# Kernel tuning notes

Measured on AMD Instinct MI355X. Metric: run time of the kernel, lower is better.

## Reference

```python
import jax, jax.numpy as jnp
import numpy as np

BN_EPS = 1e-3  # Keras BatchNormalization default epsilon


def batchnorm(x, gamma, beta):
    # axis=2 channel BN with training=True: batch stats over (batch, seq)
    m = jnp.mean(x, axis=(0, 1))
    v = jnp.var(x, axis=(0, 1))
    return gamma * (x - m) * jax.lax.rsqrt(v + BN_EPS) + beta


def setup_inputs() -> dict:
    key = jax.random.key(0)
    ks = jax.random.split(key, 8)
    B, L, Din, D, S = 8, 512, 64, 1024, 2
    s = 0.02
    return {
        "x": jax.random.normal(ks[0], (B, L, Din), jnp.float32),
        "W_embed": jax.random.normal(ks[1], (Din, D), jnp.float32) * s,
        "bn1_gamma": jnp.ones((D,), jnp.float32),
        "bn1_beta": jnp.zeros((D,), jnp.float32),
        "Wq": jax.random.normal(ks[2], (S, D, D), jnp.float32) * s,
        "bq": jnp.zeros((S, D), jnp.float32),
        "Wk": jax.random.normal(ks[3], (S, D, D), jnp.float32) * s,
        "bk": jnp.zeros((S, D), jnp.float32),
        "Wv": jax.random.normal(ks[4], (S, D, D), jnp.float32) * s,
        "bv": jnp.zeros((S, D), jnp.float32),
        "bn_gamma": jnp.ones((S, D), jnp.float32),
        "bn_beta": jnp.zeros((S, D), jnp.float32),
        "Wc1": jax.random.normal(ks[5], (S, D, D), jnp.float32) * s,
        "bc1": jnp.zeros((S, D), jnp.float32),
        "bn2_gamma": jnp.ones((S, D), jnp.float32),
        "bn2_beta": jnp.zeros((S, D), jnp.float32),
        "num_heads": 16,
    }


def reference(x, W_embed, bn1_gamma, bn1_beta, Wq, bq, Wk, bk, Wv, bv,
              bn_gamma, bn_beta, Wc1, bc1, bn2_gamma, bn2_beta, num_heads):
    # embedding: kernel-1 conv1d == matmul, then BN (training stats)
    enc = batchnorm(jnp.einsum('bli,id->bld', x, W_embed), bn1_gamma, bn1_beta)
    S = Wq.shape[0]
    B, L, D = enc.shape
    h = num_heads
    dh = D // h
    scale = 1.0 / (dh ** 0.5)
    for i in range(S):
        # relu-activated Q/K/V projections (Dense(..., activation=relu))
        q = jax.nn.relu(jnp.einsum('bld,de->ble', enc, Wq[i]) + bq[i])
        k = jax.nn.relu(jnp.einsum('bld,de->ble', enc, Wk[i]) + bk[i])
        v = jax.nn.relu(jnp.einsum('bld,de->ble', enc, Wv[i]) + bv[i])
        # split/concat head trick == reshape to [B, L, h, dh]
        qh = q.reshape(B, L, h, dh)
        kh = k.reshape(B, L, h, dh)
        vh = v.reshape(B, L, h, dh)
        scores = jnp.einsum('blhd,bmhd->bhlm', qh, kh) * scale
        attn = jax.nn.softmax(scores, axis=-1)
        out = jnp.einsum('bhlm,bmhd->blhd', attn, vh).reshape(B, L, D)
        enc = batchnorm(out + enc, bn_gamma[i], bn_beta[i])
        # feedforward: source applies conv1 TWICE (conv2 unused) — faithful
        f = jax.nn.relu(jnp.einsum('bld,de->ble', enc, Wc1[i]) + bc1[i])
        f = jax.nn.relu(jnp.einsum('bld,de->ble', f, Wc1[i]) + bc1[i])
        enc = batchnorm(f + enc, bn2_gamma[i], bn2_beta[i])
    return enc
```

## Files before the change

kernel.cpp:

```cpp
#include <hip/hip_runtime.h>
#include <hip/hip_bf16.h>
#include <cstddef>

#define D_MODEL 1024
#define M_ROWS  4096
#define BN_EPS  1e-3f
#define C_EXP2  0.18033688011112042f
#define INV_N   (1.0f / 4096.0f)

typedef __attribute__((ext_vector_type(8))) short short8;
typedef __attribute__((ext_vector_type(4))) short short4v;
typedef __attribute__((ext_vector_type(8))) unsigned short ushortx8;
typedef __attribute__((ext_vector_type(4))) float f32x4;

__device__ __forceinline__ unsigned short f2bf(float f) {
    __hip_bfloat16 h = __float2bfloat16(f);
    return *reinterpret_cast<unsigned short*>(&h);
}
__device__ __forceinline__ float bf2f(unsigned short u) {
    return __uint_as_float(((unsigned)u) << 16);
}
__device__ __forceinline__ unsigned int cvt_pk_bf16(float lo, float hi) {
    unsigned int r;
    asm volatile("v_cvt_pk_bf16_f32 %0, %1, %2" : "=v"(r) : "v"(lo), "v"(hi));
    return r;
}

template<int MODE>
__global__ __launch_bounds__(256)
void gemm_bf16_kernel(const unsigned short* __restrict__ A,
                      const unsigned short* __restrict__ Bt,
                      const float* __restrict__ b0, const float* __restrict__ b1,
                      const float* __restrict__ b2,
                      unsigned short* __restrict__ Cout,
                      const unsigned short* __restrict__ resid,
                      float* __restrict__ accp, int N, int Kd) {
    __shared__ unsigned short As[2][128 * 32];
    __shared__ unsigned short Bs[2][128 * 32];
    const int tid = threadIdx.x;
    const int lane = tid & 63;
    const int w = tid >> 6;
    const int wr = w >> 1, wc = w & 1;
    const int rowBase = blockIdx.y * 128;
    const int colBase = blockIdx.x * 128;

    const int chunk0 = w * 64 + lane;
    const int r0 = chunk0 >> 2;
    const int c0 = (chunk0 & 3) ^ ((r0 >> 1) & 3);
    const int chunk1 = 256 + chunk0;
    const int r1 = chunk1 >> 2;
    const int c1 = (chunk1 & 3) ^ ((r1 >> 1) & 3);
    const size_t aOff0 = (size_t)(rowBase + r0) * Kd + c0 * 8;
    const size_t aOff1 = (size_t)(rowBase + r1) * Kd + c1 * 8;
    const size_t bOff0 = (size_t)(colBase + r0) * Kd + c0 * 8;
    const size_t bOff1 = (size_t)(colBase + r1) * Kd + c1 * 8;
    const int ldsOff0 = (w * 64) * 8;
    const int ldsOff1 = (256 + w * 64) * 8;

    f32x4 acc[4][4];
    #pragma unroll
    for (int m = 0; m < 4; ++m)
        #pragma unroll
        for (int n = 0; n < 4; ++n)
            acc[m][n] = (f32x4){0.f, 0.f, 0.f, 0.f};

    #define STAGE(buf, kt) do {                                                   \
        const int k0_ = (kt) << 5;                                                \
        __builtin_amdgcn_global_load_lds(                                         \
            (const __attribute__((address_space(1))) void*)(A + aOff0 + k0_),     \
            (__attribute__((address_space(3))) void*)(&As[buf][ldsOff0]), 16, 0, 0);\
        __builtin_amdgcn_global_load_lds(                                         \
            (const __attribute__((address_space(1))) void*)(A + aOff1 + k0_),     \
            (__attribute__((address_space(3))) void*)(&As[buf][ldsOff1]), 16, 0, 0);\
        __builtin_amdgcn_global_load_lds(                                         \
            (const __attribute__((address_space(1))) void*)(Bt + bOff0 + k0_),    \
            (__attribute__((address_space(3))) void*)(&Bs[buf][ldsOff0]), 16, 0, 0);\
        __builtin_amdgcn_global_load_lds(                                         \
            (const __attribute__((address_space(1))) void*)(Bt + bOff1 + k0_),    \
            (__attribute__((address_space(3))) void*)(&Bs[buf][ldsOff1]), 16, 0, 0);\
    } while (0)

    const int NT = Kd >> 5;
    STAGE(0, 0);

    const int kb = lane >> 4;
    const int s = kb ^ ((lane >> 1) & 3);
    const int rA = wr * 64 + (lane & 15);
    const int rB = wc * 64 + (lane & 15);

    for (int t = 0; t < NT; ++t) {
        __syncthreads();
        if (t + 1 < NT) STAGE((t + 1) & 1, t + 1);
        const unsigned short* as = As[t & 1];
        const unsigned short* bs = Bs[t & 1];
        short8 a[4], b[4];
        #pragma unroll
        for (int m = 0; m < 4; ++m)
            a[m] = *(const short8*)&as[(rA + m * 16) * 32 + s * 8];
        #pragma unroll
        for (int n = 0; n < 4; ++n)
            b[n] = *(const short8*)&bs[(rB + n * 16) * 32 + s * 8];
        #pragma unroll
        for (int m = 0; m < 4; ++m)
            #pragma unroll
            for (int n = 0; n < 4; ++n)
                acc[m][n] = __builtin_amdgcn_mfma_f32_16x16x32_bf16(
                    a[m], b[n], acc[m][n], 0, 0, 0);
    }
    #undef STAGE

    const int cRow0 = rowBase + wr * 64 + (lane >> 4) * 4;
    const int cCol0 = colBase + wc * 64 + (lane & 15);
    float cs[4] = {}, cq[4] = {};
    #pragma unroll
    for (int n = 0; n < 4; ++n) {
        const int col = cCol0 + n * 16;
        float bv = 0.0f;
        if (MODE != 2) {
            const float* bp = (col < 1024) ? b0 : (col < 2048) ? b1 : b2;
            bv = bp[col & 1023];
        }
        #pragma unroll
        for (int m = 0; m < 4; ++m)
            #pragma unroll
            for (int r = 0; r < 4; ++r) {
                const int row = cRow0 + m * 16 + r;
                float v = acc[m][n][r];
                if (MODE != 2) v = fmaxf(v + bv, 0.0f);
                if (MODE == 1) v += bf2f(resid[(size_t)row * N + col]);
                if (MODE != 0) { cs[n] += v; cq[n] += v * v; }
                Cout[(size_t)row * N + col] = f2bf(v);
            }
    }
    if (MODE != 0) {
        #pragma unroll
        for (int n = 0; n < 4; ++n) {
            cs[n] += __shfl_xor(cs[n], 16); cs[n] += __shfl_xor(cs[n], 32);
            cq[n] += __shfl_xor(cq[n], 16); cq[n] += __shfl_xor(cq[n], 32);
        }
        if (lane < 16) {
            #pragma unroll
            for (int n = 0; n < 4; ++n) {
                const int col = colBase + wc * 64 + lane + n * 16;
                atomicAdd(&accp[col], cs[n]);
                atomicAdd(&accp[D_MODEL + col], cq[n]);
            }
        }
    }
}

__global__ __launch_bounds__(256)
void prep_weights_kernel(const float* __restrict__ Wq, const float* __restrict__ Wk,
                         const float* __restrict__ Wv, const float* __restrict__ Wc1,
                         unsigned short* __restrict__ Wtqkv,
                         unsigned short* __restrict__ Wtc1) {
    const int z = blockIdx.z;
    const int layer = z >> 2, typ = z & 3;
    const size_t wo = (size_t)layer * 1048576;
    const float* src;
    unsigned short* dst;
    if (typ == 0)      { src = Wq + wo;  dst = Wtqkv + layer * 3145728; }
    else if (typ == 1) { src = Wk + wo;  dst = Wtqkv + layer * 3145728 + 1048576; }
    else if (typ == 2) { src = Wv + wo;  dst = Wtqkv + layer * 3145728 + 2097152; }
    else               { src = Wc1 + wo; dst = Wtc1 + layer * 1048576; }
    __shared__ float T[64][65];
    const int tid = threadIdx.x;
    const int kBase = blockIdx.y * 64;
    const int nBase = blockIdx.x * 64;
    const int rr = tid >> 4;
    const int c4 = (tid & 15) * 4;
    #pragma unroll
    for (int i = 0; i < 4; ++i) {
        const int k = i * 16 + rr;
        const float4 v = *reinterpret_cast<const float4*>(
            &src[(size_t)(kBase + k) * 1024 + nBase + c4]);
        T[k][c4] = v.x; T[k][c4 + 1] = v.y; T[k][c4 + 2] = v.z; T[k][c4 + 3] = v.w;
    }
    __syncthreads();
    #pragma unroll
    for (int i = 0; i < 4; ++i) {
        const int n = i * 16 + rr;
        ushort4 o;
        o.x = f2bf(T[c4 + 0][n]); o.y = f2bf(T[c4 + 1][n]);
        o.z = f2bf(T[c4 + 2][n]); o.w = f2bf(T[c4 + 3][n]);
        *reinterpret_cast<ushort4*>(&dst[(size_t)(nBase + n) * 1024 + kBase + c4]) = o;
    }
}

__global__ __launch_bounds__(256)
void prep_misc_kernel(const float* __restrict__ x, const float* __restrict__ Wemb,
                      unsigned short* __restrict__ xbf,
                      unsigned short* __restrict__ Wembt,
                      float* __restrict__ accum) {
    const int b = blockIdx.x;
    const int tid = threadIdx.x;
    if (b < 128) {
        const size_t base = (size_t)b * 2048 + tid * 8;
        const float4 v0 = *reinterpret_cast<const float4*>(&x[base]);
        const float4 v1 = *reinterpret_cast<const float4*>(&x[base + 4]);
        ushortx8 o;
        o[0] = f2bf(v0.x); o[1] = f2bf(v0.y); o[2] = f2bf(v0.z); o[3] = f2bf(v0.w);
        o[4] = f2bf(v1.x); o[5] = f2bf(v1.y); o[6] = f2bf(v1.z); o[7] = f2bf(v1.w);
        *reinterpret_cast<ushortx8*>(&xbf[base]) = o;
    } else if (b < 144) {
        __shared__ float T[64][65];
        const int nBase = (b - 128) * 64;
        const int rr = tid >> 4;
        const int c4 = (tid & 15) * 4;
        #pragma unroll
        for (int i = 0; i < 4; ++i) {
            const int k = i * 16 + rr;
            const float4 v = *reinterpret_cast<const float4*>(
                &Wemb[(size_t)k * 1024 + nBase + c4]);
            T[k][c4] = v.x; T[k][c4 + 1] = v.y; T[k][c4 + 2] = v.z; T[k][c4 + 3] = v.w;
        }
        __syncthreads();
        #pragma unroll
        for (int i = 0; i < 4; ++i) {
            const int n = i * 16 + rr;
            ushort4 o;
            o.x = f2bf(T[c4 + 0][n]); o.y = f2bf(T[c4 + 1][n]);
            o.z = f2bf(T[c4 + 2][n]); o.w = f2bf(T[c4 + 3][n]);
            *reinterpret_cast<ushort4*>(&Wembt[(size_t)(nBase + n) * 64 + c4]) = o;
        }
    } else {
        for (int j = tid; j < 5 * 2048; j += 256) accum[j] = 0.0f;
    }
}

__global__ __launch_bounds__(256)
void attn_kernel(const unsigned short* __restrict__ QKV,
                 const unsigned short* __restrict__ Ebf,
                 unsigned short* __restrict__ Sbf,
                 float* __restrict__ accp) {
    __shared__ unsigned short Qs[128 * 64];
    __shared__ unsigned short Ks[2][64 * 64];
    __shared__ unsigned short Vt[2][64 * 72];

    const int tid = threadIdx.x;
    const int lane = tid & 63;
    const int w = tid >> 6;
    const int m = lane & 15;
    const int g = lane >> 4;
    const int l7 = lane & 7;
    const int qt = blockIdx.x, hh = blockIdx.y, bb = blockIdx.z;
    const int colB = hh * 64;
    const size_t rowQ = (size_t)bb * 512 + qt * 128;
    const size_t rowKV = (size_t)bb * 512;

    const int vk0 = (tid & 31) * 2;
    const int vcv = tid >> 5;

    #define STAGE_K(buf, kt) do {                                                  \
        const size_t kb_ = rowKV + (size_t)(kt) * 64;                              \
        _Pragma("unroll")                                                          \
        for (int i_ = 0; i_ < 2; ++i_) {                                           \
            const int c_ = w * 128 + i_ * 64 + lane;                               \
            const int r_ = c_ >> 3;                                                \
            const int gc_ = (c_ & 7) ^ (r_ & 7);                                   \
            __builtin_amdgcn_global_load_lds(                                      \
                (const __attribute__((address_space(1))) void*)                    \
                    (QKV + (kb_ + r_) * 3072 + 1024 + colB + gc_ * 8),             \
                (__attribute__((address_space(3))) void*)                          \
                    (&Ks[buf][(w * 128 + i_ * 64) * 8]), 16, 0, 0);                \
        }                                                                          \
    } while (0)

    #define LOAD_V(kt) do {                                                        \
        const size_t kb_ = rowKV + (size_t)(kt) * 64;                              \
        vst0 = *(const ushortx8*)(QKV + (kb_ + vk0) * 3072 + 2048 + colB + vcv * 8);\
        vst1 = *(const ushortx8*)(QKV + (kb_ + vk0 + 1) * 3072 + 2048 + colB + vcv * 8);\
    } while (0)

    #define WRITE_V(buf) do {                                                      \
        _Pragma("unroll")                                                          \
        for (int j_ = 0; j_ < 8; ++j_) {                                           \
            const int d_ = vcv * 8 + j_;                                           \
            unsigned int pk_ = (unsigned int)(unsigned short)vst0[j_] |            \
                               ((unsigned int)(unsigned short)vst1[j_] << 16);     \
            *(unsigned int*)&Vt[buf][d_ * 72 + vk0] = pk_;                         \
        }                                                                          \
    } while (0)

    ushortx8 vst0, vst1;

    #pragma unroll
    for (int i = 0; i < 4; ++i) {
        const int c = w * 256 + i * 64 + lane;
        const int r = c >> 3;
        const int gc = (c & 7) ^ (r & 7);
        __builtin_amdgcn_global_load_lds(
            (const __attribute__((address_space(1))) void*)
                (QKV + (rowQ + r) * 3072 + colB + gc * 8),
            (__attribute__((address_space(3))) void*)
                (&Qs[(w * 256 + i * 64) * 8]), 16, 0, 0);
    }
    STAGE_K(0, 0);
    LOAD_V(0);
    WRITE_V(0);
    __syncthreads();

    short8 qb[2][2];
    #pragma unroll
    for (int nf = 0; nf < 2; ++nf)
        #pragma unroll
        for (int ks = 0; ks < 2; ++ks)
            qb[nf][ks] = *(const short8*)&Qs[(w * 32 + 16 * nf + m) * 64 +
                                             ((g + 4 * ks) ^ l7) * 8];

    f32x4 o[2][4];
    #pragma unroll
    for (int nf = 0; nf < 2; ++nf)
        #pragma unroll
        for (int dn = 0; dn < 4; ++dn)
            o[nf][dn] = (f32x4){0.f, 0.f, 0.f, 0.f};
    float mr[2] = {-1e30f, -1e30f};
    float lsm[2] = {0.f, 0.f};

    for (int kt = 0; kt < 8; ++kt) {
        const int cur = kt & 1, nxt = cur ^ 1;
        if (kt < 7) { STAGE_K(nxt, kt + 1); LOAD_V(kt + 1); }

        f32x4 st[4][2];
        #pragma unroll
        for (int mf = 0; mf < 4; ++mf)
            #pragma unroll
            for (int nf = 0; nf < 2; ++nf)
                st[mf][nf] = (f32x4){0.f, 0.f, 0.f, 0.f};
        #pragma unroll
        for (int ks = 0; ks < 2; ++ks) {
            short8 a[4];
            #pragma unroll
            for (int mf = 0; mf < 4; ++mf)
                a[mf] = *(const short8*)&Ks[cur][(m + 16 * mf) * 64 +
                                                 ((g + 4 * ks) ^ l7) * 8];
            __builtin_amdgcn_s_setprio(1);
            #pragma unroll
            for (int mf = 0; mf < 4; ++mf)
                #pragma unroll
                for (int nf = 0; nf < 2; ++nf)
                    st[mf][nf] = __builtin_amdgcn_mfma_f32_16x16x32_bf16(
                        a[mf], qb[nf][ks], st[mf][nf], 0, 0, 0);
            __builtin_amdgcn_s_setprio(0);
        }

        float pmax[2];
        #pragma unroll
        for (int nf = 0; nf < 2; ++nf) {
            float a0 = fmaxf(fmaxf(st[0][nf][0], st[0][nf][1]),
                             fmaxf(st[0][nf][2], st[0][nf][3]));
            float a1 = fmaxf(fmaxf(st[1][nf][0], st[1][nf][1]),
                             fmaxf(st[1][nf][2], st[1][nf][3]));
            float a2 = fmaxf(fmaxf(st[2][nf][0], st[2][nf][1]),
                             fmaxf(st[2][nf][2], st[2][nf][3]));
            float a3 = fmaxf(fmaxf(st[3][nf][0], st[3][nf][1]),
                             fmaxf(st[3][nf][2], st[3][nf][3]));
            float mx = fmaxf(fmaxf(a0, a1), fmaxf(a2, a3));
            mx = fmaxf(mx, __shfl_xor(mx, 16));
            mx = fmaxf(mx, __shfl_xor(mx, 32));
            pmax[nf] = mx;
        }
        const int need = (pmax[0] - mr[0] > 64.f) || (pmax[1] - mr[1] > 64.f);
        if (__any(need)) {
            float al[2];
            #pragma unroll
            for (int nf = 0; nf < 2; ++nf) {
                const float mn = fmaxf(mr[nf], pmax[nf]);
                al[nf] = exp2f((mr[nf] - mn) * C_EXP2);
                lsm[nf] *= al[nf];
                mr[nf] = mn;
            }
            #pragma unroll
            for (int nf = 0; nf < 2; ++nf)
                #pragma unroll
                for (int r = 0; r < 4; ++r) {
                    const float av = __shfl(al[nf], 4 * g + r);
                    #pragma unroll
                    for (int dn = 0; dn < 4; ++dn)
                        o[nf][dn][r] *= av;
                }
        }

        float pf[2][4][4];
        #pragma unroll
        for (int nf = 0; nf < 2; ++nf) {
            const float mc = mr[nf] * C_EXP2;
            float s0 = 0.f, s1 = 0.f, s2 = 0.f, s3 = 0.f;
            #pragma unroll
            for (int mf = 0; mf < 4; ++mf) {
                float p0 = exp2f(fmaf(st[mf][nf][0], C_EXP2, -mc));
                float p1 = exp2f(fmaf(st[mf][nf][1], C_EXP2, -mc));
                float p2 = exp2f(fmaf(st[mf][nf][2], C_EXP2, -mc));
                float p3 = exp2f(fmaf(st[mf][nf][3], C_EXP2, -mc));
                pf[nf][mf][0] = p0; pf[nf][mf][1] = p1;
                pf[nf][mf][2] = p2; pf[nf][mf][3] = p3;
                s0 += p0; s1 += p1; s2 += p2; s3 += p3;
            }
            float ls = (s0 + s1) + (s2 + s3);
            ls += __shfl_xor(ls, 16);
            ls += __shfl_xor(ls, 32);
            lsm[nf] += ls;
        }

        if (kt < 7) WRITE_V(nxt);

        short8 pb[2][2];
        #pragma unroll
        for (int nf = 0; nf < 2; ++nf)
            #pragma unroll
            for (int ks = 0; ks < 2; ++ks) {
                union { unsigned int u[4]; short8 s; } cv;
                cv.u[0] = cvt_pk_bf16(pf[nf][2 * ks][0], pf[nf][2 * ks][1]);
                cv.u[1] = cvt_pk_bf16(pf[nf][2 * ks][2], pf[nf][2 * ks][3]);
                cv.u[2] = cvt_pk_bf16(pf[nf][2 * ks + 1][0], pf[nf][2 * ks + 1][1]);
                cv.u[3] = cvt_pk_bf16(pf[nf][2 * ks + 1][2], pf[nf][2 * ks + 1][3]);
                pb[nf][ks] = cv.s;
            }

        #pragma unroll
        for (int ks = 0; ks < 2; ++ks) {
            short8 vb[4];
            #pragma unroll
            for (int dn = 0; dn < 4; ++dn) {
                const int d = m + 16 * dn;
                const short4v lo = *(const short4v*)&Vt[cur][d * 72 + 4 * g + 32 * ks];
                const short4v hi = *(const short4v*)&Vt[cur][d * 72 + 4 * g + 16 + 32 * ks];
                vb[dn] = __builtin_shufflevector(lo, hi, 0, 1, 2, 3, 4, 5, 6, 7);
            }
            __builtin_amdgcn_s_setprio(1);
            #pragma unroll
            for (int nf = 0; nf < 2; ++nf)
                #pragma unroll
                for (int dn = 0; dn < 4; ++dn)
                    o[nf][dn] = __builtin_amdgcn_mfma_f32_16x16x32_bf16(
                        pb[nf][ks], vb[dn], o[nf][dn], 0, 0, 0);
            __builtin_amdgcn_s_setprio(0);
        }
        __syncthreads();
    }

    float cs[4] = {}, cq[4] = {};
    #pragma unroll
    for (int nf = 0; nf < 2; ++nf) {
        const float inv = 1.0f / lsm[nf];
        #pragma unroll
        for (int r = 0; r < 4; ++r) {
            const float sc = __shfl(inv, 4 * g + r);
            const size_t row = rowQ + w * 32 + 16 * nf + 4 * g + r;
            #pragma unroll
            for (int dn = 0; dn < 4; ++dn) {
                const int ch = colB + 16 * dn + m;
                const float sv = o[nf][dn][r] * sc + bf2f(Ebf[row * D_MODEL + ch]);
                Sbf[row * D_MODEL + ch] = f2bf(sv);
                cs[dn] += sv; cq[dn] += sv * sv;
            }
        }
    }
    #pragma unroll
    for (int dn = 0; dn < 4; ++dn) {
        cs[dn] += __shfl_xor(cs[dn], 16); cs[dn] += __shfl_xor(cs[dn], 32);
        cq[dn] += __shfl_xor(cq[dn], 16); cq[dn] += __shfl_xor(cq[dn], 32);
    }
    if (lane < 16) {
        #pragma unroll
        for (int dn = 0; dn < 4; ++dn) {
            atomicAdd(&accp[colB + 16 * dn + lane], cs[dn]);
            atomicAdd(&accp[D_MODEL + colB + 16 * dn + lane], cq[dn]);
        }
    }
    #undef STAGE_K
    #undef LOAD_V
    #undef WRITE_V
}

template<bool FINAL>
__global__ __launch_bounds__(256)
void bn_apply_kernel(const unsigned short* __restrict__ S,
                     const float* __restrict__ accum,
                     const float* __restrict__ gamma,
                     const float* __restrict__ beta,
                     unsigned short* __restrict__ Ebf,
                     float* __restrict__ outF) {
    const int idx = blockIdx.x * 256 + threadIdx.x;
    const int c8 = (idx & 127) << 3;
    const ushortx8 sv = *(const ushortx8*)&S[(size_t)idx * 8];
    const float4 s0 = *(const float4*)&accum[c8];
    const float4 s1 = *(const float4*)&accum[c8 + 4];
    const float4 q0 = *(const float4*)&accum[D_MODEL + c8];
    const float4 q1 = *(const float4*)&accum[D_MODEL + c8 + 4];
    const float4 g0 = *(const float4*)&gamma[c8];
    const float4 g1 = *(const float4*)&gamma[c8 + 4];
    const float4 t0 = *(const float4*)&beta[c8];
    const float4 t1 = *(const float4*)&beta[c8 + 4];
    const float ss[8] = {s0.x, s0.y, s0.z, s0.w, s1.x, s1.y, s1.z, s1.w};
    const float qq[8] = {q0.x, q0.y, q0.z, q0.w, q1.x, q1.y, q1.z, q1.w};
    const float gg[8] = {g0.x, g0.y, g0.z, g0.w, g1.x, g1.y, g1.z, g1.w};
    const float tt[8] = {t0.x, t0.y, t0.z, t0.w, t1.x, t1.y, t1.z, t1.w};
    float o[8];
    #pragma unroll
    for (int j = 0; j < 8; ++j) {
        const float mean = ss[j] * INV_N;
        const float var = qq[j] * INV_N - mean * mean;
        const float a = gg[j] * rsqrtf(var + BN_EPS);
        o[j] = fmaf(bf2f(sv[j]), a, tt[j] - mean * a);
    }
    if (FINAL) {
        *reinterpret_cast<float4*>(&outF[(size_t)idx * 8]) =
            make_float4(o[0], o[1], o[2], o[3]);
        *reinterpret_cast<float4*>(&outF[(size_t)idx * 8 + 4]) =
            make_float4(o[4], o[5], o[6], o[7]);
    } else {
        union { unsigned int u[4]; ushortx8 s; } cv;
        cv.u[0] = cvt_pk_bf16(o[0], o[1]);
        cv.u[1] = cvt_pk_bf16(o[2], o[3]);
        cv.u[2] = cvt_pk_bf16(o[4], o[5]);
        cv.u[3] = cvt_pk_bf16(o[6], o[7]);
        *reinterpret_cast<ushortx8*>(&Ebf[(size_t)idx * 8]) = cv.s;
    }
}

extern "C" void kernel_launch(void* const* d_in, const int* in_sizes, int n_in,
                              void* d_out, int out_size, void* d_ws, size_t ws_size,
                              hipStream_t stream) {
    const float* x       = (const float*)d_in[0];
    const float* W_embed = (const float*)d_in[1];
    const float* bn1_g   = (const float*)d_in[2];
    const float* bn1_b   = (const float*)d_in[3];
    const float* Wq      = (const float*)d_in[4];
    const float* bq      = (const float*)d_in[5];
    const float* Wk      = (const float*)d_in[6];
    const float* bk      = (const float*)d_in[7];
    const float* Wv      = (const float*)d_in[8];
    const float* bv      = (const float*)d_in[9];
    const float* bng     = (const float*)d_in[10];
    const float* bnb     = (const float*)d_in[11];
    const float* Wc1     = (const float*)d_in[12];
    const float* bc1     = (const float*)d_in[13];
    const float* bn2g    = (const float*)d_in[14];
    const float* bn2b    = (const float*)d_in[15];

    const size_t NBUF = (size_t)M_ROWS * D_MODEL;
    char* ws = (char*)d_ws;
    float* accum = (float*)ws;
    unsigned short* xbf   = (unsigned short*)(accum + 5 * 2048);
    unsigned short* Wembt = xbf + 262144;
    unsigned short* Ebf   = Wembt + 65536;
    unsigned short* Sbf   = Ebf + NBUF;
    unsigned short* QKVbf = Sbf + NBUF;
    unsigned short* F1bf  = QKVbf;
    unsigned short* Wtqkv = QKVbf + (size_t)M_ROWS * 3072;
    unsigned short* Wtc1  = Wtqkv + 2 * (size_t)3145728;
    float* outF = (float*)d_out;

    prep_misc_kernel<<<145, 256, 0, stream>>>(x, W_embed, xbf, Wembt, accum);
    prep_weights_kernel<<<dim3(16, 16, 8), 256, 0, stream>>>(Wq, Wk, Wv, Wc1,
                                                             Wtqkv, Wtc1);

    gemm_bf16_kernel<2><<<dim3(8, 32), 256, 0, stream>>>(
        xbf, Wembt, nullptr, nullptr, nullptr, Sbf, nullptr, accum, 1024, 64);
    bn_apply_kernel<false><<<2048, 256, 0, stream>>>(Sbf, accum, bn1_g, bn1_b,
                                                     Ebf, nullptr);

    for (int i = 0; i < 2; ++i) {
        const size_t bo = (size_t)i * D_MODEL;
        float* accA = accum + (1 + 2 * i) * 2048;
        float* accF = accum + (2 + 2 * i) * 2048;
        const unsigned short* WtqkvL = Wtqkv + (size_t)i * 3145728;
        const unsigned short* Wtc1L  = Wtc1 + (size_t)i * 1048576;

        gemm_bf16_kernel<0><<<dim3(24, 32), 256, 0, stream>>>(
            Ebf, WtqkvL, bq + bo, bk + bo, bv + bo, QKVbf, nullptr, nullptr,
            3072, 1024);
        attn_kernel<<<dim3(4, 16, 8), 256, 0, stream>>>(QKVbf, Ebf, Sbf, accA);
        bn_apply_kernel<false><<<2048, 256, 0, stream>>>(Sbf, accA, bng + bo,
                                                         bnb + bo, Ebf, nullptr);

        gemm_bf16_kernel<0><<<dim3(8, 32), 256, 0, stream>>>(
            Ebf, Wtc1L, bc1 + bo, bc1 + bo, bc1 + bo, F1bf, nullptr, nullptr,
            1024, 1024);
        gemm_bf16_kernel<1><<<dim3(8, 32), 256, 0, stream>>>(
            F1bf, Wtc1L, bc1 + bo, bc1 + bo, bc1 + bo, Sbf, Ebf, accF,
            1024, 1024);
        if (i == 0)
            bn_apply_kernel<false><<<2048, 256, 0, stream>>>(Sbf, accF, bn2g + bo,
                                                             bn2b + bo, Ebf, nullptr);
        else
            bn_apply_kernel<true><<<2048, 256, 0, stream>>>(Sbf, accF, bn2g + bo,
                                                            bn2b + bo, nullptr, outF);
    }
}
```

Measured before the change: 275.3 us.

## Use 64-row GEMM tiles for N=1024 GEMMs and merge prep kernels

Adds a gemm64 variant with 64x128 tiles so the 1024-wide GEMMs (embedding, both FFN convs) launch 512 blocks instead of 256, filling more of the MI355X's CUs. The original 128x128 kernel is specialized to the QKV path only (bias+relu). The two prep kernels are merged into one launch to save a kernel launch. Smaller tiles reduce data reuse per block and double the number of atomics for the BN statistics.

Measured after the change: 260.6 us, median of 2. 5.4% less time.

```diff
diff --git a/kernel.cpp b/kernel.cpp
--- a/kernel.cpp
+++ b/kernel.cpp
@@ -111,17 +111,113 @@
 
     const int cRow0 = rowBase + wr * 64 + (lane >> 4) * 4;
     const int cCol0 = colBase + wc * 64 + (lane & 15);
+    #pragma unroll
+    for (int n = 0; n < 4; ++n) {
+        const int col = cCol0 + n * 16;
+        const float* bp = (col < 1024) ? b0 : (col < 2048) ? b1 : b2;
+        const float bv = bp[col & 1023];
+        #pragma unroll
+        for (int m = 0; m < 4; ++m)
+            #pragma unroll
+            for (int r = 0; r < 4; ++r) {
+                const int row = cRow0 + m * 16 + r;
+                const float v = fmaxf(acc[m][n][r] + bv, 0.0f);
+                Cout[(size_t)row * N + col] = f2bf(v);
+            }
+    }
+}
+
+template<int MODE>
+__global__ __launch_bounds__(256)
+void gemm64_bf16_kernel(const unsigned short* __restrict__ A,
+                        const unsigned short* __restrict__ Bt,
+                        const float* __restrict__ bias,
+                        unsigned short* __restrict__ Cout,
+                        const unsigned short* __restrict__ resid,
+                        float* __restrict__ accp, int N, int Kd) {
+    __shared__ unsigned short As[2][64 * 32];
+    __shared__ unsigned short Bs[2][128 * 32];
+    const int tid = threadIdx.x;
+    const int lane = tid & 63;
+    const int w = tid >> 6;
+    const int wr = w >> 1, wc = w & 1;
+    const int rowBase = blockIdx.y * 64;
+    const int colBase = blockIdx.x * 128;
+
+    const int ra = tid >> 2;
+    const int ca = (tid & 3) ^ ((ra >> 1) & 3);
+    const size_t aOff = (size_t)(rowBase + ra) * Kd + ca * 8;
+    const int chunk0 = w * 64 + lane;
+    const int r0 = chunk0 >> 2;
+    const int c0 = (chunk0 & 3) ^ ((r0 >> 1) & 3);
+    const int chunk1 = 256 + chunk0;
+    const int r1 = chunk1 >> 2;
+    const int c1 = (chunk1 & 3) ^ ((r1 >> 1) & 3);
+    const size_t bOff0 = (size_t)(colBase + r0) * Kd + c0 * 8;
+    const size_t bOff1 = (size_t)(colBase + r1) * Kd + c1 * 8;
+    const int ldsA = (w * 64) * 8;
+    const int ldsB0 = (w * 64) * 8;
+    const int ldsB1 = (256 + w * 64) * 8;
+
+    f32x4 acc[2][4];
+    #pragma unroll
+    for (int m = 0; m < 2; ++m)
+        #pragma unroll
+        for (int n = 0; n < 4; ++n)
+            acc[m][n] = (f32x4){0.f, 0.f, 0.f, 0.f};
+
+    #define STAGE(buf, kt) do {                                                   \
+        const int k0_ = (kt) << 5;                                                \
+        __builtin_amdgcn_global_load_lds(                                         \
+            (const __attribute__((address_space(1))) void*)(A + aOff + k0_),      \
+            (__attribute__((address_space(3))) void*)(&As[buf][ldsA]), 16, 0, 0); \
+        __builtin_amdgcn_global_load_lds(                                         \
+            (const __attribute__((address_space(1))) void*)(Bt + bOff0 + k0_),    \
+            (__attribute__((address_space(3))) void*)(&Bs[buf][ldsB0]), 16, 0, 0);\
+        __builtin_amdgcn_global_load_lds(                                         \
+            (const __attribute__((address_space(1))) void*)(Bt + bOff1 + k0_),    \
+            (__attribute__((address_space(3))) void*)(&Bs[buf][ldsB1]), 16, 0, 0);\
+    } while (0)
+
+    const int NT = Kd >> 5;
+    STAGE(0, 0);
+
+    const int kb = lane >> 4;
+    const int s = kb ^ ((lane >> 1) & 3);
+    const int rA = wr * 32 + (lane & 15);
+    const int rB = wc * 64 + (lane & 15);
+
+    for (int t = 0; t < NT; ++t) {
+        __syncthreads();
+        if (t + 1 < NT) STAGE((t + 1) & 1, t + 1);
+        const unsigned short* as = As[t & 1];
+        const unsigned short* bs = Bs[t & 1];
+        short8 a[2], b[4];
+        #pragma unroll
+        for (int m = 0; m < 2; ++m)
+            a[m] = *(const short8*)&as[(rA + m * 16) * 32 + s * 8];
+        #pragma unroll
+        for (int n = 0; n < 4; ++n)
+            b[n] = *(const short8*)&bs[(rB + n * 16) * 32 + s * 8];
+        #pragma unroll
+        for (int m = 0; m < 2; ++m)
+            #pragma unroll
+            for (int n = 0; n < 4; ++n)
+                acc[m][n] = __builtin_amdgcn_mfma_f32_16x16x32_bf16(
+                    a[m], b[n], acc[m][n], 0, 0, 0);
+    }
+    #undef STAGE
+
+    const int cRow0 = rowBase + wr * 32 + (lane >> 4) * 4;
+    const int cCol0 = colBase + wc * 64 + (lane & 15);
     float cs[4] = {}, cq[4] = {};
     #pragma unroll
     for (int n = 0; n < 4; ++n) {
         const int col = cCol0 + n * 16;
         float bv = 0.0f;
-        if (MODE != 2) {
-            const float* bp = (col < 1024) ? b0 : (col < 2048) ? b1 : b2;
-            bv = bp[col & 1023];
-        }
-        #pragma unroll
-        for (int m = 0; m < 4; ++m)
+        if (MODE != 2) bv = bias[col & 1023];
+        #pragma unroll
+        for (int m = 0; m < 2; ++m)
             #pragma unroll
             for (int r = 0; r < 4; ++r) {
                 const int row = cRow0 + m * 16 + r;
@@ -150,50 +246,47 @@
 }
 
 __global__ __launch_bounds__(256)
-void prep_weights_kernel(const float* __restrict__ Wq, const float* __restrict__ Wk,
-                         const float* __restrict__ Wv, const float* __restrict__ Wc1,
-                         unsigned short* __restrict__ Wtqkv,
-                         unsigned short* __restrict__ Wtc1) {
+void prep_kernel(const float* __restrict__ Wq, const float* __restrict__ Wk,
+                 const float* __restrict__ Wv, const float* __restrict__ Wc1,
+                 const float* __restrict__ x, const float* __restrict__ Wemb,
+                 unsigned short* __restrict__ Wtqkv, unsigned short* __restrict__ Wtc1,
+                 unsigned short* __restrict__ xbf, unsigned short* __restrict__ Wembt,
+                 float* __restrict__ accum) {
     const int z = blockIdx.z;
-    const int layer = z >> 2, typ = z & 3;
-    const size_t wo = (size_t)layer * 1048576;
-    const float* src;
-    unsigned short* dst;
-    if (typ == 0)      { src = Wq + wo;  dst = Wtqkv + layer * 3145728; }
-    else if (typ == 1) { src = Wk + wo;  dst = Wtqkv + layer * 3145728 + 1048576; }
-    else if (typ == 2) { src = Wv + wo;  dst = Wtqkv + layer * 3145728 + 2097152; }
-    else               { src = Wc1 + wo; dst = Wtc1 + layer * 1048576; }
-    __shared__ float T[64][65];
     const int tid = threadIdx.x;
-    const int kBase = blockIdx.y * 64;
-    const int nBase = blockIdx.x * 64;
-    const int rr = tid >> 4;
-    const int c4 = (tid & 15) * 4;
-    #pragma unroll
-    for (int i = 0; i < 4; ++i) {
-        const int k = i * 16 + rr;
-        const float4 v = *reinterpret_cast<const float4*>(
-            &src[(size_t)(kBase + k) * 1024 + nBase + c4]);
-        T[k][c4] = v.x; T[k][c4 + 1] = v.y; T[k][c4 + 2] = v.z; T[k][c4 + 3] = v.w;
-    }
-    __syncthreads();
-    #pragma unroll
-    for (int i = 0; i < 4; ++i) {
-        const int n = i * 16 + rr;
-        ushort4 o;
-        o.x = f2bf(T[c4 + 0][n]); o.y = f2bf(T[c4 + 1][n]);
-        o.z = f2bf(T[c4 + 2][n]); o.w = f2bf(T[c4 + 3][n]);
-        *reinterpret_cast<ushort4*>(&dst[(size_t)(nBase + n) * 1024 + kBase + c4]) = o;
-    }
-}
-
-__global__ __launch_bounds__(256)
-void prep_misc_kernel(const float* __restrict__ x, const float* __restrict__ Wemb,
-                      unsigned short* __restrict__ xbf,
-                      unsigned short* __restrict__ Wembt,
-                      float* __restrict__ accum) {
-    const int b = blockIdx.x;
-    const int tid = threadIdx.x;
+    if (z < 8) {
+        const int layer = z >> 2, typ = z & 3;
+        const size_t wo = (size_t)layer * 1048576;
+        const float* src;
+        unsigned short* dst;
+        if (typ == 0)      { src = Wq + wo;  dst = Wtqkv + layer * 3145728; }
+        else if (typ == 1) { src = Wk + wo;  dst = Wtqkv + layer * 3145728 + 1048576; }
+        else if (typ == 2) { src = Wv + wo;  dst = Wtqkv + layer * 3145728 + 2097152; }
+        else               { src = Wc1 + wo; dst = Wtc1 + layer * 1048576; }
+        __shared__ float T[64][65];
+        const int kBase = blockIdx.y * 64;
+        const int nBase = blockIdx.x * 64;
+        const int rr = tid >> 4;
+        const int c4 = (tid & 15) * 4;
+        #pragma unroll
+        for (int i = 0; i < 4; ++i) {
+            const int k = i * 16 + rr;
+            const float4 v = *reinterpret_cast<const float4*>(
+                &src[(size_t)(kBase + k) * 1024 + nBase + c4]);
+            T[k][c4] = v.x; T[k][c4 + 1] = v.y; T[k][c4 + 2] = v.z; T[k][c4 + 3] = v.w;
+        }
+        __syncthreads();
+        #pragma unroll
+        for (int i = 0; i < 4; ++i) {
+            const int n = i * 16 + rr;
+            ushort4 o;
+            o.x = f2bf(T[c4 + 0][n]); o.y = f2bf(T[c4 + 1][n]);
+            o.z = f2bf(T[c4 + 2][n]); o.w = f2bf(T[c4 + 3][n]);
+            *reinterpret_cast<ushort4*>(&dst[(size_t)(nBase + n) * 1024 + kBase + c4]) = o;
+        }
+        return;
+    }
+    const int b = blockIdx.y * 16 + blockIdx.x;
     if (b < 128) {
         const size_t base = (size_t)b * 2048 + tid * 8;
         const float4 v0 = *reinterpret_cast<const float4*>(&x[base]);
@@ -223,7 +316,7 @@
             o.z = f2bf(T[c4 + 2][n]); o.w = f2bf(T[c4 + 3][n]);
             *reinterpret_cast<ushort4*>(&Wembt[(size_t)(nBase + n) * 64 + c4]) = o;
         }
-    } else {
+    } else if (b == 144) {
         for (int j = tid; j < 5 * 2048; j += 256) accum[j] = 0.0f;
     }
 }
@@ -552,12 +645,11 @@
     unsigned short* Wtc1  = Wtqkv + 2 * (size_t)3145728;
     float* outF = (float*)d_out;
 
-    prep_misc_kernel<<<145, 256, 0, stream>>>(x, W_embed, xbf, Wembt, accum);
-    prep_weights_kernel<<<dim3(16, 16, 8), 256, 0, stream>>>(Wq, Wk, Wv, Wc1,
-                                                             Wtqkv, Wtc1);
-
-    gemm_bf16_kernel<2><<<dim3(8, 32), 256, 0, stream>>>(
-        xbf, Wembt, nullptr, nullptr, nullptr, Sbf, nullptr, accum, 1024, 64);
+    prep_kernel<<<dim3(16, 16, 9), 256, 0, stream>>>(
+        Wq, Wk, Wv, Wc1, x, W_embed, Wtqkv, Wtc1, xbf, Wembt, accum);
+
+    gemm64_bf16_kernel<2><<<dim3(8, 64), 256, 0, stream>>>(
+        xbf, Wembt, nullptr, Sbf, nullptr, accum, 1024, 64);
     bn_apply_kernel<false><<<2048, 256, 0, stream>>>(Sbf, accum, bn1_g, bn1_b,
                                                      Ebf, nullptr);
 
@@ -575,12 +667,10 @@
         bn_apply_kernel<false><<<2048, 256, 0, stream>>>(Sbf, accA, bng + bo,
                                                          bnb + bo, Ebf, nullptr);
 
-        gemm_bf16_kernel<0><<<dim3(8, 32), 256, 0, stream>>>(
-            Ebf, Wtc1L, bc1 + bo, bc1 + bo, bc1 + bo, F1bf, nullptr, nullptr,
-            1024, 1024);
-        gemm_bf16_kernel<1><<<dim3(8, 32), 256, 0, stream>>>(
-            F1bf, Wtc1L, bc1 + bo, bc1 + bo, bc1 + bo, Sbf, Ebf, accF,
-            1024, 1024);
+        gemm64_bf16_kernel<0><<<dim3(8, 64), 256, 0, stream>>>(
+            Ebf, Wtc1L, bc1 + bo, F1bf, nullptr, nullptr, 1024, 1024);
+        gemm64_bf16_kernel<1><<<dim3(8, 64), 256, 0, stream>>>(
+            F1bf, Wtc1L, bc1 + bo, Sbf, Ebf, accF, 1024, 1024);
         if (i == 0)
             bn_apply_kernel<false><<<2048, 256, 0, stream>>>(Sbf, accF, bn2g + bo,
                                                              bn2b + bo, Ebf, nullptr);
```
